# Performance work log

Measured on AMD Instinct MI355X. Metric: run time of the kernel, lower is better.

The kernel has to match this reference:

```python
import jax, jax.numpy as jnp
import numpy as np


def setup_inputs() -> dict:
    key = jax.random.key(0)
    k1, k2 = jax.random.split(key)
    B, C, KX, KZ = 512, 256, 6, 22
    x = jax.random.normal(k1, (B, C, KX, KX), dtype=jnp.float32)  # exemplar (kernel)
    z = jax.random.normal(k2, (B, C, KZ, KZ), dtype=jnp.float32)  # search region (input)
    return {"x": x, "z": z}


def reference(x, z):
    # Per-sample cross-correlation: out[b] = conv2d(z[b], x[b]) (valid, stride 1).
    # Expressed as a single grouped convolution with groups=B instead of a
    # Python loop of B separate conv2d calls.
    B, C, kz, _ = z.shape
    z2 = z.reshape(1, B * C, kz, kz)              # [1, B*C, kz, kz]
    out = jax.lax.conv_general_dilated(
        z2, x,
        window_strides=(1, 1),
        padding="VALID",
        dimension_numbers=("NCHW", "OIHW", "NCHW"),
        feature_group_count=B,
    )                                              # [1, B, ho, wo]
    return jnp.transpose(out, (1, 0, 2, 3))        # [B, 1, ho, wo]
```

## Files before the change

kernel.cpp:

```cpp
#include <hip/hip_runtime.h>
#include <cstdint>
#include <cstddef>

#define BB      512
#define CC      256
#define KXX     6
#define KZZ     22
#define HO      17
#define OUTHW   (HO * HO)
#define ZCH     (KZZ * KZZ)
#define XCH     (KXX * KXX)

#define CHUNK_C   8
#define NCHUNK    (CC / CHUNK_C)
#define ZCHUNK    (CHUNK_C * ZCH)
#define XCHUNK    (CHUNK_C * XCH)
#define NT        320
#define NBUF      3

typedef const __attribute__((address_space(1))) void* gptr_t;
typedef __attribute__((address_space(3))) void* lptr_t;

#define WAITVM(N) asm volatile("s_waitcnt vmcnt(" #N ")" ::: "memory")

__device__ __forceinline__ void cp16_async(void* lds_base, const void* gsrc) {
  __builtin_amdgcn_global_load_lds((gptr_t)gsrc, (lptr_t)lds_base, 16, 0, 0);
}
__device__ __forceinline__ void cp4_async(void* lds_base, const void* gsrc) {
  __builtin_amdgcn_global_load_lds((gptr_t)gsrc, (lptr_t)lds_base, 4, 0, 0);
}

__device__ __forceinline__ void stage_chunk(float* zdst, float* xdst,
                                            const float* zsrc, const float* xsrc,
                                            int wave, int lane) {
  char* zd = (char*)zdst;
  const char* zs = (const char*)zsrc;
#pragma unroll
  for (int i = 0; i < 3; ++i) {
    const int grp = wave * 3 + i;
    cp16_async(zd + grp * 1024, zs + grp * 1024 + lane * 16);
  }
  if (wave == 0) {
    if (lane < 32) cp4_async(zd + 15360, zs + 15360 + lane * 4);
  } else if (wave == 1) {
    cp16_async((char*)xdst, (const char*)xsrc + lane * 16);
  } else if (wave == 2) {
    if (lane < 32) cp4_async((char*)xdst + 1024, (const char*)xsrc + 1024 + lane * 4);
  }
}

__global__ __launch_bounds__(NT, 2) void corr_kernel(const float* __restrict__ x,
                                                     const float* __restrict__ z,
                                                     float* __restrict__ out) {
  __shared__ __align__(16) float zbuf[NBUF][ZCHUNK];
  __shared__ __align__(16) float xbuf[NBUF][XCHUNK];

  const int b    = blockIdx.x;
  const int t    = threadIdx.x;
  const int wave = t >> 6;
  const int lane = t & 63;

  const float* zb = z + (size_t)b * (CC * ZCH);
  const float* xb = x + (size_t)b * (CC * XCH);

  stage_chunk(zbuf[0], xbuf[0], zb, xb, wave, lane);
  stage_chunk(zbuf[1], xbuf[1], zb + ZCHUNK, xb + XCHUNK, wave, lane);
  stage_chunk(zbuf[2], xbuf[2], zb + 2 * ZCHUNK, xb + 2 * XCHUNK, wave, lane);

  const int  g      = t / 17;
  const int  oy     = t - g * 17;
  const int  cl     = g & 7;
  const int  kyh    = g >> 3;
  const bool active = (g < 16);

  float acc[HO];
#pragma unroll
  for (int i = 0; i < HO; ++i) acc[i] = 0.0f;

  for (int k = 0; k < NCHUNK; ++k) {
    const int buf = k % 3;

    const int rem = NCHUNK - 1 - k;
    if (rem >= 2) {
      if (wave < 3) WAITVM(8); else WAITVM(6);
    } else if (rem == 1) {
      if (wave < 3) WAITVM(4); else WAITVM(3);
    } else {
      WAITVM(0);
    }
    __builtin_amdgcn_s_barrier();

    if (active) {
      const float* zc = &zbuf[buf][cl * ZCH];
      const float* xc = &xbuf[buf][cl * XCH + kyh * (3 * KXX)];

      __align__(16) float xv[3 * KXX];
#pragma unroll
      for (int i = 0; i < 9; ++i)
        ((float2*)xv)[i] = ((const float2*)xc)[i];

#pragma unroll
      for (int ky2 = 0; ky2 < 3; ++ky2) {
        const int row = oy + kyh * 3 + ky2;
        const float* zr = zc + row * KZZ;
        __align__(16) float zv[KZZ + 1];
#pragma unroll
        for (int i = 0; i < 11; ++i)
          ((float2*)zv)[i] = ((const float2*)zr)[i];
#pragma unroll
        for (int kx = 0; kx < KXX; ++kx) {
          const float xs = xv[ky2 * KXX + kx];
#pragma unroll
          for (int ox = 0; ox < HO; ++ox)
            acc[ox] = fmaf(zv[ox + kx], xs, acc[ox]);
        }
      }
    }

    __builtin_amdgcn_s_barrier();
    if (k + 3 < NCHUNK)
      stage_chunk(zbuf[buf], xbuf[buf],
                  zb + (size_t)(k + 3) * ZCHUNK, xb + (size_t)(k + 3) * XCHUNK,
                  wave, lane);
  }

  __syncthreads();
  float* red = &zbuf[0][0];
  if (active) {
#pragma unroll
    for (int ox = 0; ox < HO; ++ox)
      red[g * OUTHW + oy * HO + ox] = acc[ox];
  }
  __syncthreads();
  if (t < OUTHW) {
    float s = 0.0f;
#pragma unroll
    for (int gg = 0; gg < 16; ++gg) s += red[gg * OUTHW + t];
    out[(size_t)b * OUTHW + t] = s;
  }
}

extern "C" void kernel_launch(void* const* d_in, const int* in_sizes, int n_in,
                              void* d_out, int out_size, void* d_ws, size_t ws_size,
                              hipStream_t stream) {
  const float* x = (const float*)d_in[0];
  const float* z = (const float*)d_in[1];
  float* out = (float*)d_out;
  corr_kernel<<<BB, NT, 0, stream>>>(x, z, out);
}
```

Measured before the change: 400.6 us.

## Use dedicated producer wave with 4-deep LDS ring and single barrier per chunk

Adds a sixth wave that only issues async global-to-LDS copies, using a 4-buffer ring with prefetch distance 2. The per-chunk second barrier is dropped, and the compute waves no longer issue loads. This is meant to overlap loads with FMA work and cut barrier overhead. The cost is more LDS, which may reduce occupancy, plus one wave that does no compute. The producer's vmcnt-based waits must also stay correct.

Result: faster. 365.9 us (-8.7%).

```diff
diff --git a/kernel.cpp b/kernel.cpp
--- a/kernel.cpp
+++ b/kernel.cpp
@@ -15,8 +15,9 @@
 #define NCHUNK    (CC / CHUNK_C)
 #define ZCHUNK    (CHUNK_C * ZCH)
 #define XCHUNK    (CHUNK_C * XCH)
-#define NT        320
-#define NBUF      3
+#define NT        384
+#define PRODW     5
+#define NBUF      4
 
 typedef const __attribute__((address_space(1))) void* gptr_t;
 typedef __attribute__((address_space(3))) void* lptr_t;
@@ -30,23 +31,17 @@
   __builtin_amdgcn_global_load_lds((gptr_t)gsrc, (lptr_t)lds_base, 4, 0, 0);
 }
 
-__device__ __forceinline__ void stage_chunk(float* zdst, float* xdst,
-                                            const float* zsrc, const float* xsrc,
-                                            int wave, int lane) {
+__device__ __forceinline__ void stage_chunk_1w(float* zdst, float* xdst,
+                                               const float* zsrc, const float* xsrc,
+                                               int lane) {
   char* zd = (char*)zdst;
   const char* zs = (const char*)zsrc;
 #pragma unroll
-  for (int i = 0; i < 3; ++i) {
-    const int grp = wave * 3 + i;
-    cp16_async(zd + grp * 1024, zs + grp * 1024 + lane * 16);
-  }
-  if (wave == 0) {
-    if (lane < 32) cp4_async(zd + 15360, zs + 15360 + lane * 4);
-  } else if (wave == 1) {
-    cp16_async((char*)xdst, (const char*)xsrc + lane * 16);
-  } else if (wave == 2) {
-    if (lane < 32) cp4_async((char*)xdst + 1024, (const char*)xsrc + 1024 + lane * 4);
-  }
+  for (int i = 0; i < 15; ++i)
+    cp16_async(zd + i * 1024, zs + i * 1024 + lane * 16);
+  if (lane < 32) cp4_async(zd + 15360, zs + 15360 + lane * 4);
+  cp16_async((char*)xdst, (const char*)xsrc + lane * 16);
+  if (lane < 32) cp4_async((char*)xdst + 1024, (const char*)xsrc + 1024 + lane * 4);
 }
 
 __global__ __launch_bounds__(NT, 2) void corr_kernel(const float* __restrict__ x,
@@ -63,14 +58,15 @@
   const float* zb = z + (size_t)b * (CC * ZCH);
   const float* xb = x + (size_t)b * (CC * XCH);
 
-  stage_chunk(zbuf[0], xbuf[0], zb, xb, wave, lane);
-  stage_chunk(zbuf[1], xbuf[1], zb + ZCHUNK, xb + XCHUNK, wave, lane);
-  stage_chunk(zbuf[2], xbuf[2], zb + 2 * ZCHUNK, xb + 2 * XCHUNK, wave, lane);
+  if (wave == PRODW) {
+    stage_chunk_1w(zbuf[0], xbuf[0], zb, xb, lane);
+    stage_chunk_1w(zbuf[1], xbuf[1], zb + ZCHUNK, xb + XCHUNK, lane);
+  }
 
   const int  g      = t / 17;
   const int  oy     = t - g * 17;
   const int  cl     = g & 7;
-  const int  kyh    = g >> 3;
+  const int  kyh    = (g >> 3) & 1;
   const bool active = (g < 16);
 
   float acc[HO];
@@ -78,17 +74,23 @@
   for (int i = 0; i < HO; ++i) acc[i] = 0.0f;
 
   for (int k = 0; k < NCHUNK; ++k) {
-    const int buf = k % 3;
+    const int buf = k & 3;
 
-    const int rem = NCHUNK - 1 - k;
-    if (rem >= 2) {
-      if (wave < 3) WAITVM(8); else WAITVM(6);
-    } else if (rem == 1) {
-      if (wave < 3) WAITVM(4); else WAITVM(3);
+    if (wave == PRODW) {
+      if (k + 2 < NCHUNK) {
+        stage_chunk_1w(zbuf[(k + 2) & 3], xbuf[(k + 2) & 3],
+                       zb + (size_t)(k + 2) * ZCHUNK,
+                       xb + (size_t)(k + 2) * XCHUNK, lane);
+        WAITVM(36);
+      } else if (k + 2 == NCHUNK) {
+        WAITVM(18);
+      } else {
+        WAITVM(0);
+      }
+      __builtin_amdgcn_s_barrier();
     } else {
-      WAITVM(0);
+      __syncthreads();
     }
-    __builtin_amdgcn_s_barrier();
 
     if (active) {
       const float* zc = &zbuf[buf][cl * ZCH];
@@ -116,12 +118,6 @@
         }
       }
     }
-
-    __builtin_amdgcn_s_barrier();
-    if (k + 3 < NCHUNK)
-      stage_chunk(zbuf[buf], xbuf[buf],
-                  zb + (size_t)(k + 3) * ZCHUNK, xb + (size_t)(k + 3) * XCHUNK,
-                  wave, lane);
   }
 
   __syncthreads();
```
